# Kernel optimization log

Measured on AMD Instinct MI355X. Metric: run time of the kernel, lower is better.

The kernel has to match this reference:

```python
import jax, jax.numpy as jnp
import numpy as np

C = 0.01          # ToPoincare curvature hardcoded in get_dist
K = 5             # k_way (s0..s4 hardcoded in source)
N = 5             # n_shot
Q = 15            # queries per class -> LQ = K*Q = 75
D = 1024          # feature dim (hardcoded reshape(1,-1,1024))
TEMP = 1.0
N_AUG = 40
MIN_NORM = 1e-5


def _artanh(x):
    return jnp.arctanh(jnp.clip(x, -1 + 1e-5, 1 - 1e-5))


def _project(x, c):
    norm = jnp.maximum(jnp.linalg.norm(x, axis=-1, keepdims=True), MIN_NORM)
    maxnorm = (1 - 1e-3) / jnp.sqrt(c)
    return jnp.where(norm > maxnorm, x / norm * maxnorm, x)


def _expmap0(u, c):
    sc = jnp.sqrt(c)
    un = jnp.maximum(jnp.linalg.norm(u, axis=-1, keepdims=True), MIN_NORM)
    return jnp.tanh(sc * un) * u / (sc * un)


def _mobius_add(x, y, c):
    x2 = jnp.sum(x * x, -1, keepdims=True)
    y2 = jnp.sum(y * y, -1, keepdims=True)
    xy = jnp.sum(x * y, -1, keepdims=True)
    num = (1 + 2 * c * xy + c * y2) * x + (1 - c * x2) * y
    den = 1 + 2 * c * xy + c * c * x2 * y2
    return num / jnp.maximum(den, MIN_NORM)


def _expmap(x, u, c):
    # exp map at point x of tangent vector u
    sc = jnp.sqrt(c)
    un = jnp.maximum(jnp.linalg.norm(u, axis=-1, keepdims=True), MIN_NORM)
    lam = 2.0 / jnp.maximum(1 - c * jnp.sum(x * x, -1, keepdims=True), MIN_NORM)
    second = jnp.tanh(sc * lam * un / 2) * u / (sc * un)
    return _mobius_add(x, second, c)


def _ptransp0_p(x, v, c):
    # parallel transport of v from the origin to x
    return v * (1 - c * jnp.sum(x * x, -1, keepdims=True))


def _dist_matrix(x, y, c):
    # pairwise Poincare distance [n, m] without materializing [n,m,d]:
    # ||(-x) (+) y||^2 = a^2 x2 + b^2 y2 - 2ab<x,y>, a = 1-2c<x,y>+c y2, b = 1-c x2
    sc = jnp.sqrt(c)
    x2 = jnp.sum(x * x, -1)[:, None]
    y2 = jnp.sum(y * y, -1)[None, :]
    xy = x @ y.T
    a = 1 - 2 * c * xy + c * y2
    b = 1 - c * x2
    num2 = a * a * x2 + b * b * y2 - 2 * a * b * xy
    den = 1 - 2 * c * xy + c * c * x2 * y2
    norm = jnp.sqrt(jnp.maximum(num2, 0.0)) / jnp.maximum(den, MIN_NORM)
    return 2.0 / sc * _artanh(sc * norm)


def _p2k(x, c):
    return 2 * x / (1 + c * jnp.sum(x * x, -1, keepdims=True))


def _k2p(x, c):
    return x / (1 + jnp.sqrt(jnp.maximum(1 - c * jnp.sum(x * x, -1, keepdims=True), 0.0)))


def _poincare_mean_masked(x, mask, c):
    # Einstein-midpoint Poincare mean over rows of x weighted by {0,1} mask
    k = _p2k(x, c)
    lam = 1.0 / jnp.sqrt(jnp.maximum(1 - c * jnp.sum(k * k, -1), MIN_NORM))
    w = lam * mask
    mean_k = (w[:, None] * k).sum(0) / w.sum()
    return _k2p(mean_k, c)


def setup_inputs() -> dict:
    key = jax.random.key(0)
    k1, k2, k3 = jax.random.split(key, 3)
    feat = jax.random.normal(k1, (K * N + K * Q, D), dtype=jnp.float32)
    label = jax.random.randint(k2, (2, K * Q), 0, K)
    noise = jax.random.normal(k3, (K, N_AUG, D), dtype=jnp.float32)
    return {"feat": feat, "label": label, "noise": noise}


def reference(feat, label, noise):
    support_e = feat[: N * K].reshape(K, N, D)
    queries_e = feat[N * K:]                                  # [LQ, D]
    support_p_ = _project(_expmap0(feat[: N * K], C), C).reshape(K, N, D)
    queries_p = _project(_expmap0(queries_e, C), C)           # [LQ, D]

    ones_n = jnp.ones((N,), feat.dtype)
    proto_p = jax.vmap(lambda s: _poincare_mean_masked(s, ones_n, C))(support_p_)  # [K, D]
    dist = _dist_matrix(queries_p, proto_p, C) / TEMP          # [LQ, K]
    pred = jnp.argmax(-dist, 1)                                # [LQ]
    qmask = (pred[:, None] == jnp.arange(K)[None, :]).astype(feat.dtype)  # [LQ, K]

    def per_class(sup_p, sup_e, mq, nz):
        # sup_p/sup_e: [N,D]; mq: [LQ] routing mask; nz: [N_AUG,D] unit normals
        m = jnp.concatenate([ones_n, mq])                      # [N+LQ]
        pts_p = jnp.concatenate([sup_p, queries_p], 0)
        pts_e = jnp.concatenate([sup_e, queries_e], 0)
        s_p = _poincare_mean_masked(pts_p, m, C)               # [D] augmented proto
        cnt = m.sum()
        mu = (m[:, None] * pts_e).sum(0) / cnt
        var = (m[:, None] * (pts_e - mu) ** 2).sum(0) / (cnt - 1)  # unbiased, as torch.std
        std = jnp.sqrt(var)                                    # [D]
        v = nz * std                                           # torch.normal(0, std), 40 samples
        pt = _ptransp0_p(s_p[None, :], v, C)
        ex = _expmap(s_p[None, :], pt, C)                      # [N_AUG, D]
        s_new = jnp.concatenate([sup_p, ex], 0)                # [N+N_AUG, D]
        return _poincare_mean_masked(s_new, jnp.ones((N + N_AUG,), feat.dtype), C)

    proto_new = jax.vmap(per_class, in_axes=(0, 0, 1, 0))(support_p_, support_e, qmask, noise)
    dist_new = _dist_matrix(queries_p, proto_new, C) / TEMP

    y_pred = jax.nn.softmax(-dist_new, axis=1)
    log_p_y = jax.nn.log_softmax(-dist, axis=1)
    # nn.CrossEntropyLoss applied to log-probs (double log-softmax, faithful to source)
    ll = jax.nn.log_softmax(log_p_y, axis=1)
    lbl = label[1]
    loss = -jnp.mean(jnp.take_along_axis(ll, lbl[:, None], axis=1))
    return y_pred, loss
```

## Files before the change

### kernel.cpp

```cpp
#include <hip/hip_runtime.h>
#include <hip/hip_bf16.h>
#include <math.h>

#define CCd     0.01
#define SCd     0.1
#define MAXNRMd 9.99
#define MINNd   1e-5
#define DD      1024
#define NK      25
#define NQ      75
#define NROWS   100
#define KCLS    5
#define NAUG    40

__device__ __forceinline__ double wave_reduce_d(double v){
#pragma unroll
  for (int o = 32; o > 0; o >>= 1) v += __shfl_xor(v, o);
  return v;
}

__device__ __forceinline__ double hyp_dist_d(double xy, double x2, double y2){
  double a    = 1.0 - 2.0*CCd*xy + CCd*y2;
  double b    = 1.0 - CCd*x2;
  double num2 = a*a*x2 + b*b*y2 - 2.0*a*b*xy;
  double den  = 1.0 - 2.0*CCd*xy + CCd*CCd*x2*y2;
  double nrm  = sqrt(fmax(num2, 0.0)) / fmax(den, MINNd);
  double z    = SCd * nrm;
  z = fmin(fmax(z, -1.0 + MINNd), 1.0 - MINNd);
  return 10.0 * log((1.0 + z) / (1.0 - z));
}

__device__ __forceinline__ void kweights(double pp, double* la, double* l_out){
  double a  = 2.0/(1.0 + CCd*pp);
  double k2 = a*a*pp;
  double l  = 1.0/sqrt(fmax(1.0 - CCd*k2, MINNd));
  *la = l*a; *l_out = l;
}

__global__ __launch_bounds__(256)
void k_expmap(const float* __restrict__ feat, float* __restrict__ P,
              double* __restrict__ p2d){
  const int r = blockIdx.x, t = threadIdx.x;
  const float4 v = reinterpret_cast<const float4*>(feat + r*DD)[t];
  double ss = (double)v.x*v.x + (double)v.y*v.y + (double)v.z*v.z + (double)v.w*v.w;
  __shared__ double red[4];
  ss = wave_reduce_d(ss);
  if ((t & 63) == 0) red[t >> 6] = ss;
  __syncthreads();
  ss = red[0] + red[1] + red[2] + red[3];
  double un = fmax(sqrt(ss), MINNd);
  double th = tanh(SCd*un);
  double na = th * 10.0;
  double factor, pn;
  if (na > MAXNRMd) { factor = MAXNRMd/un; pn = MAXNRMd; }
  else              { factor = th/(SCd*un); pn = na; }
  float4 o;
  o.x = (float)(v.x*factor); o.y = (float)(v.y*factor);
  o.z = (float)(v.z*factor); o.w = (float)(v.w*factor);
  reinterpret_cast<float4*>(P + r*DD)[t] = o;
  if (t == 0) p2d[r] = pn*pn;
}

__global__ __launch_bounds__(1024)
void k_proto(const float* __restrict__ P, const double* __restrict__ p2d,
             float* __restrict__ protoP, double* __restrict__ proto2d){
  const int c = blockIdx.x, t = threadIdx.x;
  double la[5], wsum = 0.0;
#pragma unroll
  for (int i = 0; i < 5; i++){
    double lam;
    kweights(p2d[c*5+i], &la[i], &lam);
    wsum += lam;
  }
  double s = 0.0;
#pragma unroll
  for (int i = 0; i < 5; i++) s += la[i]*(double)P[(c*5+i)*DD + t];
  s /= wsum;
  __shared__ double red[16];
  double ss = wave_reduce_d(s*s);
  if ((t & 63) == 0) red[t >> 6] = ss;
  __syncthreads();
  ss = 0.0;
#pragma unroll
  for (int i = 0; i < 16; i++) ss += red[i];
  double sf = 1.0/(1.0 + sqrt(fmax(1.0 - CCd*ss, 0.0)));
  protoP[c*DD + t] = (float)(s*sf);
  if (t == 0) proto2d[c] = ss*sf*sf;
}

__global__ __launch_bounds__(256)
void k_dist1(const float* __restrict__ P, const float* __restrict__ protoP,
             const double* __restrict__ p2d, const double* __restrict__ proto2d,
             double* __restrict__ distS, int* __restrict__ predS){
  const int q = blockIdx.x, t = threadIdx.x;
  const float* xq = P + (NK+q)*DD;
  double acc[5] = {0,0,0,0,0};
#pragma unroll
  for (int k = 0; k < 4; k++){
    int d = t + 256*k;
    double x = (double)xq[d];
#pragma unroll
    for (int c = 0; c < 5; c++) acc[c] += x*(double)protoP[c*DD + d];
  }
  __shared__ double red[4][5];
#pragma unroll
  for (int c = 0; c < 5; c++) acc[c] = wave_reduce_d(acc[c]);
  if ((t & 63) == 0){
#pragma unroll
    for (int c = 0; c < 5; c++) red[t >> 6][c] = acc[c];
  }
  __syncthreads();
  if (t == 0){
    double x2 = p2d[NK+q];
    double best = 1e300; int bi = 0;
#pragma unroll
    for (int c = 0; c < 5; c++){
      double dot = red[0][c] + red[1][c] + red[2][c] + red[3][c];
      double dv  = hyp_dist_d(dot, x2, proto2d[c]);
      distS[q*5 + c] = dv;
      if (dv < best){ best = dv; bi = c; }
    }
    predS[q] = bi;
  }
}

__global__ __launch_bounds__(256)
void k_stats(const float* __restrict__ feat, const float* __restrict__ P,
             const double* __restrict__ p2d, const int* __restrict__ predS,
             double* __restrict__ std_g, double* __restrict__ mkr_g,
             double* __restrict__ mk2part){
  const int c = blockIdx.x >> 2, chunk = blockIdx.x & 3, t = threadIdx.x;
  __shared__ double wA[80], wL[80], wM[80], scal[2], red[4];
  __shared__ int rows[80];
  if (t < 80){
    int row; double m;
    if (t < 5){ row = c*5 + t; m = 1.0; }
    else      { row = NK + (t-5); m = (predS[t-5] == c) ? 1.0 : 0.0; }
    rows[t] = row;
    double la, l; kweights(p2d[row], &la, &l);
    wA[t] = m*la; wL[t] = m*l; wM[t] = m;
  }
  __syncthreads();
  if (t == 0){
    double wsum = 0.0, cnt = 0.0;
    for (int i = 0; i < 80; i++){ wsum += wL[i]; cnt += wM[i]; }
    scal[0] = wsum; scal[1] = cnt;
  }
  __syncthreads();
  const double wsum = scal[0], cnt = scal[1];
  const int d = chunk*256 + t;
  double mkd = 0.0, mud = 0.0, sqd = 0.0;
  for (int i = 0; i < 80; i++){
    int row = rows[i];
    mkd += wA[i]*(double)P[row*DD + d];
    double e = (double)feat[row*DD + d];
    mud += wM[i]*e;
    sqd += wM[i]*e*e;
  }
  mkd /= wsum;
  mud /= cnt;
  double var = (sqd - cnt*mud*mud)/(cnt - 1.0);
  std_g[c*DD + d] = sqrt(fmax(var, 0.0));
  mkr_g[c*DD + d] = mkd;
  double s = wave_reduce_d(mkd*mkd);
  if ((t & 63) == 0) red[t >> 6] = s;
  __syncthreads();
  if (t == 0) mk2part[blockIdx.x] = red[0] + red[1] + red[2] + red[3];
}

__global__ __launch_bounds__(256)
void k_coef(const float* __restrict__ noise, const double* __restrict__ std_g,
            const double* __restrict__ mkr_g, const double* __restrict__ mk2part,
            double* __restrict__ coefS_g, double* __restrict__ coefV_g,
            double* __restrict__ lamJ_g){
  const int j = blockIdx.x, c = blockIdx.y, t = threadIdx.x;
  const float*  nzr = noise + (c*NAUG + j)*DD;
  const double* st  = std_g + c*DD;
  const double* mk  = mkr_g + c*DD;
  double un2 = 0.0, rd = 0.0;
#pragma unroll
  for (int k = 0; k < 4; k++){
    int d = t + 256*k;
    double v = (double)nzr[d]*st[d];
    un2 += v*v;
    rd  += v*mk[d];
  }
  __shared__ double red[4][2];
  un2 = wave_reduce_d(un2);
  rd  = wave_reduce_d(rd);
  if ((t & 63) == 0){ red[t >> 6][0] = un2; red[t >> 6][1] = rd; }
  __syncthreads();
  if (t == 0){
    double s_un2 = red[0][0]+red[1][0]+red[2][0]+red[3][0];
    double rdot  = red[0][1]+red[1][1]+red[2][1]+red[3][1];
    double mk2 = mk2part[c*4+0]+mk2part[c*4+1]+mk2part[c*4+2]+mk2part[c*4+3];
    double sf  = 1.0/(1.0 + sqrt(fmax(1.0 - CCd*mk2, 0.0)));
    double sp2 = mk2*sf*sf;
    double lamx = 2.0/fmax(1.0 - CCd*sp2, MINNd);
    double ptf  = 1.0 - CCd*sp2;
    double s_dot = sf*rdot;
    double unv = sqrt(s_un2);
    double unp = fmax(ptf*unv, MINNd);
    double g0  = tanh(SCd*lamx*unp*0.5)/(SCd*unp);
    double g   = g0*ptf;
    double y2  = g*g*s_un2;
    double xy  = g*s_dot;
    double A   = 1.0 + 2.0*CCd*xy + CCd*y2;
    double B   = ptf;
    double den = fmax(1.0 + 2.0*CCd*xy + CCd*CCd*sp2*y2, MINNd);
    double ex2 = (A*A*sp2 + 2.0*A*B*g*s_dot + B*B*g*g*s_un2)/(den*den);
    double ae  = 2.0/(1.0 + CCd*ex2);
    double k2e = ae*ae*ex2;
    double le  = 1.0/sqrt(fmax(1.0 - CCd*k2e, MINNd));
    coefS_g[c*NAUG + j] = le*ae*A/den;
    coefV_g[c*NAUG + j] = le*ae*B*g/den;
    lamJ_g[c*NAUG + j]  = le;
  }
}

__global__ __launch_bounds__(256)
void k_asm(const float* __restrict__ noise, const float* __restrict__ P,
           const double* __restrict__ p2d, const double* __restrict__ std_g,
           const double* __restrict__ mkr_g, const double* __restrict__ mk2part,
           const double* __restrict__ coefS_g, const double* __restrict__ coefV_g,
           const double* __restrict__ lamJ_g,
           float* __restrict__ protoNr, double* __restrict__ mk2Np){
  const int c = blockIdx.x >> 2, chunk = blockIdx.x & 3, t = threadIdx.x;
  __shared__ double cV[NAUG], supC[5], scal[3], red[4];
  if (t < NAUG) cV[t] = coefV_g[c*NAUG + t];
  if (t == 0){
    double lsum = 0.0, sS = 0.0;
#pragma unroll
    for (int i = 0; i < 5; i++){
      double la, l; kweights(p2d[c*5+i], &la, &l);
      supC[i] = la; lsum += l;
    }
    for (int j = 0; j < NAUG; j++){ lsum += lamJ_g[c*NAUG+j]; sS += coefS_g[c*NAUG+j]; }
    double mk2 = mk2part[c*4+0]+mk2part[c*4+1]+mk2part[c*4+2]+mk2part[c*4+3];
    double sf  = 1.0/(1.0 + sqrt(fmax(1.0 - CCd*mk2, 0.0)));
    scal[0] = lsum; scal[1] = sS; scal[2] = sf;
  }
  __syncthreads();
  const int d = chunk*256 + t;
  double val = scal[1]*scal[2]*mkr_g[c*DD + d];
#pragma unroll
  for (int i = 0; i < 5; i++) val += supC[i]*(double)P[(c*5+i)*DD + d];
  double na = 0.0;
  for (int j = 0; j < NAUG; j++) na += cV[j]*(double)noise[(c*NAUG + j)*DD + d];
  val += std_g[c*DD + d]*na;
  val /= scal[0];
  protoNr[c*DD + d] = (float)val;
  double s = wave_reduce_d(val*val);
  if ((t & 63) == 0) red[t >> 6] = s;
  __syncthreads();
  if (t == 0) mk2Np[blockIdx.x] = red[0] + red[1] + red[2] + red[3];
}

__global__ __launch_bounds__(256)
void k_dist2(const float* __restrict__ P, const float* __restrict__ protoNr,
             const double* __restrict__ p2d, const double* __restrict__ mk2Np,
             const double* __restrict__ distS, const int* __restrict__ label,
             float* __restrict__ out, double* __restrict__ lossQ){
  const int q = blockIdx.x, t = threadIdx.x;
  const float* xq = P + (NK+q)*DD;
  double acc[5] = {0,0,0,0,0};
#pragma unroll
  for (int k = 0; k < 4; k++){
    int d = t + 256*k;
    double x = (double)xq[d];
#pragma unroll
    for (int c = 0; c < 5; c++) acc[c] += x*(double)protoNr[c*DD + d];
  }
  __shared__ double red[4][5];
#pragma unroll
  for (int c = 0; c < 5; c++) acc[c] = wave_reduce_d(acc[c]);
  if ((t & 63) == 0){
#pragma unroll
    for (int c = 0; c < 5; c++) red[t >> 6][c] = acc[c];
  }
  __syncthreads();
  if (t == 0){
    double x2 = p2d[NK+q];
    double v[5]; double mx = -1e300;
#pragma unroll
    for (int c = 0; c < 5; c++){
      double mk2N = mk2Np[c*4+0]+mk2Np[c*4+1]+mk2Np[c*4+2]+mk2Np[c*4+3];
      double sfN  = 1.0/(1.0 + sqrt(fmax(1.0 - CCd*mk2N, 0.0)));
      double dot  = sfN*(red[0][c] + red[1][c] + red[2][c] + red[3][c]);
      double y2   = mk2N*sfN*sfN;
      v[c] = -hyp_dist_d(dot, x2, y2);
      mx = fmax(mx, v[c]);
    }
    double se = 0.0;
#pragma unroll
    for (int c = 0; c < 5; c++){ v[c] = exp(v[c]-mx); se += v[c]; }
    double inv = 1.0/se;
#pragma unroll
    for (int c = 0; c < 5; c++) out[q*5 + c] = (float)(v[c]*inv);

    double u[5]; mx = -1e300;
#pragma unroll
    for (int c = 0; c < 5; c++){ u[c] = -distS[q*5+c]; mx = fmax(mx, u[c]); }
    double s1 = 0.0;
#pragma unroll
    for (int c = 0; c < 5; c++) s1 += exp(u[c]-mx);
    double lse1 = mx + log(s1);
#pragma unroll
    for (int c = 0; c < 5; c++) u[c] -= lse1;
    double mx2 = -1e300;
#pragma unroll
    for (int c = 0; c < 5; c++) mx2 = fmax(mx2, u[c]);
    double s2 = 0.0;
#pragma unroll
    for (int c = 0; c < 5; c++) s2 += exp(u[c]-mx2);
    double lse2 = mx2 + log(s2);
    lossQ[q] = u[label[NQ + q]] - lse2;
  }
}

__global__ __launch_bounds__(128)
void k_loss(const double* __restrict__ lossQ, float* __restrict__ out){
  const int t = threadIdx.x;
  double v = (t < NQ) ? lossQ[t] : 0.0;
  v = wave_reduce_d(v);
  __shared__ double red[2];
  if ((t & 63) == 0) red[t >> 6] = v;
  __syncthreads();
  if (t == 0) out[NQ*KCLS] = (float)(-(red[0]+red[1])/75.0);
}

extern "C" void kernel_launch(void* const* d_in, const int* in_sizes, int n_in,
                              void* d_out, int out_size, void* d_ws, size_t ws_size,
                              hipStream_t stream) {
  const float* feat  = (const float*)d_in[0];
  const int*   label = (const int*)d_in[1];
  const float* noise = (const float*)d_in[2];
  float* out = (float*)d_out;

  float*  P        = (float*)d_ws;
  float*  protoP   = P + NROWS*DD;
  float*  protoNr  = protoP + KCLS*DD;
  double* p2d      = (double*)(protoNr + KCLS*DD);
  double* proto2d  = p2d + NROWS;
  double* distS    = proto2d + KCLS;
  double* lossQ    = distS + NQ*KCLS;
  double* std_g    = lossQ + NQ;
  double* mkr_g    = std_g + KCLS*DD;
  double* mk2part  = mkr_g + KCLS*DD;
  double* coefS_g  = mk2part + 4*KCLS;
  double* coefV_g  = coefS_g + KCLS*NAUG;
  double* lamJ_g   = coefV_g + KCLS*NAUG;
  double* mk2Np    = lamJ_g + KCLS*NAUG;
  int*    predS    = (int*)(mk2Np + 4*KCLS);

  k_expmap<<<NROWS, 256, 0, stream>>>(feat, P, p2d);
  k_proto <<<KCLS, 1024, 0, stream>>>(P, p2d, protoP, proto2d);
  k_dist1 <<<NQ, 256, 0, stream>>>(P, protoP, p2d, proto2d, distS, predS);
  k_stats <<<4*KCLS, 256, 0, stream>>>(feat, P, p2d, predS, std_g, mkr_g, mk2part);
  k_coef  <<<dim3(NAUG, KCLS), 256, 0, stream>>>(noise, std_g, mkr_g, mk2part,
                                                 coefS_g, coefV_g, lamJ_g);
  k_asm   <<<4*KCLS, 256, 0, stream>>>(noise, P, p2d, std_g, mkr_g, mk2part,
                                       coefS_g, coefV_g, lamJ_g, protoNr, mk2Np);
  k_dist2 <<<NQ, 256, 0, stream>>>(P, protoNr, p2d, mk2Np, distS, label, out, lossQ);
  k_loss  <<<1, 128, 0, stream>>>(lossQ, out);
}
```

Baseline: 98.29 us.

## Fuse all stages into one cooperative kernel with grid syncs

Replaces the eight separate kernel launches with a single cooperative kernel of 200 blocks that runs each stage in turn, separated by grid.sync(). The prototype computation is also folded into the first distance stage: each query block recomputes the class means and their norms instead of reading a stored prototype. This removes launch overhead and inter-kernel gaps. In exchange it adds grid-wide barrier cost, redundant prototype work in every query block, and a dependence on all 200 blocks being co-resident.

```diff
diff --git a/kernel.cpp b/kernel.cpp
--- a/kernel.cpp
+++ b/kernel.cpp
@@ -1,6 +1,8 @@
 #include <hip/hip_runtime.h>
-#include <hip/hip_bf16.h>
+#include <hip/hip_cooperative_groups.h>
 #include <math.h>
+
+namespace cg = cooperative_groups;
 
 #define CCd     0.01
 #define SCd     0.1
@@ -12,6 +14,7 @@
 #define NROWS   100
 #define KCLS    5
 #define NAUG    40
+#define GRIDB   200
 
 __device__ __forceinline__ double wave_reduce_d(double v){
 #pragma unroll
@@ -38,295 +41,286 @@
 }
 
 __global__ __launch_bounds__(256)
-void k_expmap(const float* __restrict__ feat, float* __restrict__ P,
-              double* __restrict__ p2d){
-  const int r = blockIdx.x, t = threadIdx.x;
-  const float4 v = reinterpret_cast<const float4*>(feat + r*DD)[t];
-  double ss = (double)v.x*v.x + (double)v.y*v.y + (double)v.z*v.z + (double)v.w*v.w;
-  __shared__ double red[4];
-  ss = wave_reduce_d(ss);
-  if ((t & 63) == 0) red[t >> 6] = ss;
-  __syncthreads();
-  ss = red[0] + red[1] + red[2] + red[3];
-  double un = fmax(sqrt(ss), MINNd);
-  double th = tanh(SCd*un);
-  double na = th * 10.0;
-  double factor, pn;
-  if (na > MAXNRMd) { factor = MAXNRMd/un; pn = MAXNRMd; }
-  else              { factor = th/(SCd*un); pn = na; }
-  float4 o;
-  o.x = (float)(v.x*factor); o.y = (float)(v.y*factor);
-  o.z = (float)(v.z*factor); o.w = (float)(v.w*factor);
-  reinterpret_cast<float4*>(P + r*DD)[t] = o;
-  if (t == 0) p2d[r] = pn*pn;
-}
-
-__global__ __launch_bounds__(1024)
-void k_proto(const float* __restrict__ P, const double* __restrict__ p2d,
-             float* __restrict__ protoP, double* __restrict__ proto2d){
-  const int c = blockIdx.x, t = threadIdx.x;
-  double la[5], wsum = 0.0;
-#pragma unroll
-  for (int i = 0; i < 5; i++){
-    double lam;
-    kweights(p2d[c*5+i], &la[i], &lam);
-    wsum += lam;
-  }
-  double s = 0.0;
-#pragma unroll
-  for (int i = 0; i < 5; i++) s += la[i]*(double)P[(c*5+i)*DD + t];
-  s /= wsum;
-  __shared__ double red[16];
-  double ss = wave_reduce_d(s*s);
-  if ((t & 63) == 0) red[t >> 6] = ss;
-  __syncthreads();
-  ss = 0.0;
-#pragma unroll
-  for (int i = 0; i < 16; i++) ss += red[i];
-  double sf = 1.0/(1.0 + sqrt(fmax(1.0 - CCd*ss, 0.0)));
-  protoP[c*DD + t] = (float)(s*sf);
-  if (t == 0) proto2d[c] = ss*sf*sf;
-}
-
-__global__ __launch_bounds__(256)
-void k_dist1(const float* __restrict__ P, const float* __restrict__ protoP,
-             const double* __restrict__ p2d, const double* __restrict__ proto2d,
-             double* __restrict__ distS, int* __restrict__ predS){
-  const int q = blockIdx.x, t = threadIdx.x;
-  const float* xq = P + (NK+q)*DD;
-  double acc[5] = {0,0,0,0,0};
-#pragma unroll
-  for (int k = 0; k < 4; k++){
-    int d = t + 256*k;
-    double x = (double)xq[d];
-#pragma unroll
-    for (int c = 0; c < 5; c++) acc[c] += x*(double)protoP[c*DD + d];
-  }
-  __shared__ double red[4][5];
-#pragma unroll
-  for (int c = 0; c < 5; c++) acc[c] = wave_reduce_d(acc[c]);
-  if ((t & 63) == 0){
-#pragma unroll
-    for (int c = 0; c < 5; c++) red[t >> 6][c] = acc[c];
-  }
-  __syncthreads();
-  if (t == 0){
-    double x2 = p2d[NK+q];
-    double best = 1e300; int bi = 0;
+void k_fused(const float* __restrict__ feat, const int* __restrict__ label,
+             const float* __restrict__ noise, float* __restrict__ out,
+             float* __restrict__ wsf)
+{
+  cg::grid_group grid = cg::this_grid();
+  const int bid = blockIdx.x, t = threadIdx.x;
+  const int lane = t & 63, wv = t >> 6;
+
+  float*  P       = wsf;
+  float*  protoNr = P + NROWS*DD;
+  double* p2d     = (double*)(protoNr + KCLS*DD);
+  double* distS   = p2d + NROWS;
+  double* lossQ   = distS + NQ*KCLS;
+  double* std_g   = lossQ + NQ;
+  double* mkr_g   = std_g + KCLS*DD;
+  double* mk2part = mkr_g + KCLS*DD;
+  double* coefS_g = mk2part + 32;
+  double* coefV_g = coefS_g + KCLS*NAUG;
+  double* lamJ_g  = coefV_g + KCLS*NAUG;
+  double* mk2Np   = lamJ_g + KCLS*NAUG;
+  int*    predS   = (int*)(mk2Np + 32);
+
+  __shared__ double redA[4];
+  __shared__ double redB[4][10];
+  __shared__ double sWA[80], sWL[80], sWM[80];
+  __shared__ int    sRows[80];
+  __shared__ double sScal[4];
+  __shared__ double redD[4][2];
+  __shared__ double sCV[NAUG], sSup[5];
+  __shared__ double redF[4][5];
+
+  if (bid < NROWS){
+    const int r = bid;
+    const float4 v = reinterpret_cast<const float4*>(feat + r*DD)[t];
+    double ss = (double)v.x*v.x + (double)v.y*v.y + (double)v.z*v.z + (double)v.w*v.w;
+    ss = wave_reduce_d(ss);
+    if (lane == 0) redA[wv] = ss;
+    __syncthreads();
+    ss = redA[0] + redA[1] + redA[2] + redA[3];
+    double un = fmax(sqrt(ss), MINNd);
+    double th = tanh(SCd*un);
+    double na = th * 10.0;
+    double factor, pn;
+    if (na > MAXNRMd) { factor = MAXNRMd/un; pn = MAXNRMd; }
+    else              { factor = th/(SCd*un); pn = na; }
+    float4 o;
+    o.x = (float)(v.x*factor); o.y = (float)(v.y*factor);
+    o.z = (float)(v.z*factor); o.w = (float)(v.w*factor);
+    reinterpret_cast<float4*>(P + r*DD)[t] = o;
+    if (t == 0) p2d[r] = pn*pn;
+  }
+  grid.sync();
+
+  if (bid < NQ){
+    const int q = bid;
+    const float* xq = P + (NK+q)*DD;
+    double ss[5], rd[5];
 #pragma unroll
     for (int c = 0; c < 5; c++){
-      double dot = red[0][c] + red[1][c] + red[2][c] + red[3][c];
-      double dv  = hyp_dist_d(dot, x2, proto2d[c]);
-      distS[q*5 + c] = dv;
-      if (dv < best){ best = dv; bi = c; }
-    }
-    predS[q] = bi;
-  }
-}
-
-__global__ __launch_bounds__(256)
-void k_stats(const float* __restrict__ feat, const float* __restrict__ P,
-             const double* __restrict__ p2d, const int* __restrict__ predS,
-             double* __restrict__ std_g, double* __restrict__ mkr_g,
-             double* __restrict__ mk2part){
-  const int c = blockIdx.x >> 2, chunk = blockIdx.x & 3, t = threadIdx.x;
-  __shared__ double wA[80], wL[80], wM[80], scal[2], red[4];
-  __shared__ int rows[80];
-  if (t < 80){
-    int row; double m;
-    if (t < 5){ row = c*5 + t; m = 1.0; }
-    else      { row = NK + (t-5); m = (predS[t-5] == c) ? 1.0 : 0.0; }
-    rows[t] = row;
-    double la, l; kweights(p2d[row], &la, &l);
-    wA[t] = m*la; wL[t] = m*l; wM[t] = m;
-  }
-  __syncthreads();
-  if (t == 0){
-    double wsum = 0.0, cnt = 0.0;
-    for (int i = 0; i < 80; i++){ wsum += wL[i]; cnt += wM[i]; }
-    scal[0] = wsum; scal[1] = cnt;
-  }
-  __syncthreads();
-  const double wsum = scal[0], cnt = scal[1];
-  const int d = chunk*256 + t;
-  double mkd = 0.0, mud = 0.0, sqd = 0.0;
-  for (int i = 0; i < 80; i++){
-    int row = rows[i];
-    mkd += wA[i]*(double)P[row*DD + d];
-    double e = (double)feat[row*DD + d];
-    mud += wM[i]*e;
-    sqd += wM[i]*e*e;
-  }
-  mkd /= wsum;
-  mud /= cnt;
-  double var = (sqd - cnt*mud*mud)/(cnt - 1.0);
-  std_g[c*DD + d] = sqrt(fmax(var, 0.0));
-  mkr_g[c*DD + d] = mkd;
-  double s = wave_reduce_d(mkd*mkd);
-  if ((t & 63) == 0) red[t >> 6] = s;
-  __syncthreads();
-  if (t == 0) mk2part[blockIdx.x] = red[0] + red[1] + red[2] + red[3];
-}
-
-__global__ __launch_bounds__(256)
-void k_coef(const float* __restrict__ noise, const double* __restrict__ std_g,
-            const double* __restrict__ mkr_g, const double* __restrict__ mk2part,
-            double* __restrict__ coefS_g, double* __restrict__ coefV_g,
-            double* __restrict__ lamJ_g){
-  const int j = blockIdx.x, c = blockIdx.y, t = threadIdx.x;
-  const float*  nzr = noise + (c*NAUG + j)*DD;
-  const double* st  = std_g + c*DD;
-  const double* mk  = mkr_g + c*DD;
-  double un2 = 0.0, rd = 0.0;
-#pragma unroll
-  for (int k = 0; k < 4; k++){
-    int d = t + 256*k;
-    double v = (double)nzr[d]*st[d];
-    un2 += v*v;
-    rd  += v*mk[d];
-  }
-  __shared__ double red[4][2];
-  un2 = wave_reduce_d(un2);
-  rd  = wave_reduce_d(rd);
-  if ((t & 63) == 0){ red[t >> 6][0] = un2; red[t >> 6][1] = rd; }
-  __syncthreads();
-  if (t == 0){
-    double s_un2 = red[0][0]+red[1][0]+red[2][0]+red[3][0];
-    double rdot  = red[0][1]+red[1][1]+red[2][1]+red[3][1];
-    double mk2 = mk2part[c*4+0]+mk2part[c*4+1]+mk2part[c*4+2]+mk2part[c*4+3];
-    double sf  = 1.0/(1.0 + sqrt(fmax(1.0 - CCd*mk2, 0.0)));
-    double sp2 = mk2*sf*sf;
-    double lamx = 2.0/fmax(1.0 - CCd*sp2, MINNd);
-    double ptf  = 1.0 - CCd*sp2;
-    double s_dot = sf*rdot;
-    double unv = sqrt(s_un2);
-    double unp = fmax(ptf*unv, MINNd);
-    double g0  = tanh(SCd*lamx*unp*0.5)/(SCd*unp);
-    double g   = g0*ptf;
-    double y2  = g*g*s_un2;
-    double xy  = g*s_dot;
-    double A   = 1.0 + 2.0*CCd*xy + CCd*y2;
-    double B   = ptf;
-    double den = fmax(1.0 + 2.0*CCd*xy + CCd*CCd*sp2*y2, MINNd);
-    double ex2 = (A*A*sp2 + 2.0*A*B*g*s_dot + B*B*g*g*s_un2)/(den*den);
-    double ae  = 2.0/(1.0 + CCd*ex2);
-    double k2e = ae*ae*ex2;
-    double le  = 1.0/sqrt(fmax(1.0 - CCd*k2e, MINNd));
-    coefS_g[c*NAUG + j] = le*ae*A/den;
-    coefV_g[c*NAUG + j] = le*ae*B*g/den;
-    lamJ_g[c*NAUG + j]  = le;
-  }
-}
-
-__global__ __launch_bounds__(256)
-void k_asm(const float* __restrict__ noise, const float* __restrict__ P,
-           const double* __restrict__ p2d, const double* __restrict__ std_g,
-           const double* __restrict__ mkr_g, const double* __restrict__ mk2part,
-           const double* __restrict__ coefS_g, const double* __restrict__ coefV_g,
-           const double* __restrict__ lamJ_g,
-           float* __restrict__ protoNr, double* __restrict__ mk2Np){
-  const int c = blockIdx.x >> 2, chunk = blockIdx.x & 3, t = threadIdx.x;
-  __shared__ double cV[NAUG], supC[5], scal[3], red[4];
-  if (t < NAUG) cV[t] = coefV_g[c*NAUG + t];
-  if (t == 0){
-    double lsum = 0.0, sS = 0.0;
-#pragma unroll
-    for (int i = 0; i < 5; i++){
-      double la, l; kweights(p2d[c*5+i], &la, &l);
-      supC[i] = la; lsum += l;
-    }
-    for (int j = 0; j < NAUG; j++){ lsum += lamJ_g[c*NAUG+j]; sS += coefS_g[c*NAUG+j]; }
-    double mk2 = mk2part[c*4+0]+mk2part[c*4+1]+mk2part[c*4+2]+mk2part[c*4+3];
-    double sf  = 1.0/(1.0 + sqrt(fmax(1.0 - CCd*mk2, 0.0)));
-    scal[0] = lsum; scal[1] = sS; scal[2] = sf;
-  }
-  __syncthreads();
-  const int d = chunk*256 + t;
-  double val = scal[1]*scal[2]*mkr_g[c*DD + d];
-#pragma unroll
-  for (int i = 0; i < 5; i++) val += supC[i]*(double)P[(c*5+i)*DD + d];
-  double na = 0.0;
-  for (int j = 0; j < NAUG; j++) na += cV[j]*(double)noise[(c*NAUG + j)*DD + d];
-  val += std_g[c*DD + d]*na;
-  val /= scal[0];
-  protoNr[c*DD + d] = (float)val;
-  double s = wave_reduce_d(val*val);
-  if ((t & 63) == 0) red[t >> 6] = s;
-  __syncthreads();
-  if (t == 0) mk2Np[blockIdx.x] = red[0] + red[1] + red[2] + red[3];
-}
-
-__global__ __launch_bounds__(256)
-void k_dist2(const float* __restrict__ P, const float* __restrict__ protoNr,
-             const double* __restrict__ p2d, const double* __restrict__ mk2Np,
-             const double* __restrict__ distS, const int* __restrict__ label,
-             float* __restrict__ out, double* __restrict__ lossQ){
-  const int q = blockIdx.x, t = threadIdx.x;
-  const float* xq = P + (NK+q)*DD;
-  double acc[5] = {0,0,0,0,0};
-#pragma unroll
-  for (int k = 0; k < 4; k++){
-    int d = t + 256*k;
-    double x = (double)xq[d];
-#pragma unroll
-    for (int c = 0; c < 5; c++) acc[c] += x*(double)protoNr[c*DD + d];
-  }
-  __shared__ double red[4][5];
-#pragma unroll
-  for (int c = 0; c < 5; c++) acc[c] = wave_reduce_d(acc[c]);
-  if ((t & 63) == 0){
-#pragma unroll
-    for (int c = 0; c < 5; c++) red[t >> 6][c] = acc[c];
-  }
-  __syncthreads();
-  if (t == 0){
-    double x2 = p2d[NK+q];
-    double v[5]; double mx = -1e300;
-#pragma unroll
-    for (int c = 0; c < 5; c++){
-      double mk2N = mk2Np[c*4+0]+mk2Np[c*4+1]+mk2Np[c*4+2]+mk2Np[c*4+3];
-      double sfN  = 1.0/(1.0 + sqrt(fmax(1.0 - CCd*mk2N, 0.0)));
-      double dot  = sfN*(red[0][c] + red[1][c] + red[2][c] + red[3][c]);
-      double y2   = mk2N*sfN*sfN;
-      v[c] = -hyp_dist_d(dot, x2, y2);
-      mx = fmax(mx, v[c]);
-    }
-    double se = 0.0;
-#pragma unroll
-    for (int c = 0; c < 5; c++){ v[c] = exp(v[c]-mx); se += v[c]; }
-    double inv = 1.0/se;
-#pragma unroll
-    for (int c = 0; c < 5; c++) out[q*5 + c] = (float)(v[c]*inv);
-
-    double u[5]; mx = -1e300;
-#pragma unroll
-    for (int c = 0; c < 5; c++){ u[c] = -distS[q*5+c]; mx = fmax(mx, u[c]); }
-    double s1 = 0.0;
-#pragma unroll
-    for (int c = 0; c < 5; c++) s1 += exp(u[c]-mx);
-    double lse1 = mx + log(s1);
-#pragma unroll
-    for (int c = 0; c < 5; c++) u[c] -= lse1;
-    double mx2 = -1e300;
-#pragma unroll
-    for (int c = 0; c < 5; c++) mx2 = fmax(mx2, u[c]);
-    double s2 = 0.0;
-#pragma unroll
-    for (int c = 0; c < 5; c++) s2 += exp(u[c]-mx2);
-    double lse2 = mx2 + log(s2);
-    lossQ[q] = u[label[NQ + q]] - lse2;
-  }
-}
-
-__global__ __launch_bounds__(128)
-void k_loss(const double* __restrict__ lossQ, float* __restrict__ out){
-  const int t = threadIdx.x;
-  double v = (t < NQ) ? lossQ[t] : 0.0;
-  v = wave_reduce_d(v);
-  __shared__ double red[2];
-  if ((t & 63) == 0) red[t >> 6] = v;
-  __syncthreads();
-  if (t == 0) out[NQ*KCLS] = (float)(-(red[0]+red[1])/75.0);
+      double la[5], wsum = 0.0;
+#pragma unroll
+      for (int i = 0; i < 5; i++){
+        double lv; kweights(p2d[c*5+i], &la[i], &lv); wsum += lv;
+      }
+      double ssc = 0.0, rdc = 0.0;
+#pragma unroll
+      for (int k = 0; k < 4; k++){
+        int d = t + 256*k;
+        double s = 0.0;
+#pragma unroll
+        for (int i = 0; i < 5; i++) s += la[i]*(double)P[(c*5+i)*DD + d];
+        s /= wsum;
+        ssc += s*s; rdc += s*(double)xq[d];
+      }
+      ss[c] = wave_reduce_d(ssc);
+      rd[c] = wave_reduce_d(rdc);
+    }
+    if (lane == 0){
+#pragma unroll
+      for (int c = 0; c < 5; c++){ redB[wv][c] = ss[c]; redB[wv][5+c] = rd[c]; }
+    }
+    __syncthreads();
+    if (t == 0){
+      double x2 = p2d[NK+q];
+      double best = 1e300; int bi = 0;
+#pragma unroll
+      for (int c = 0; c < 5; c++){
+        double sst = redB[0][c]+redB[1][c]+redB[2][c]+redB[3][c];
+        double rdt = redB[0][5+c]+redB[1][5+c]+redB[2][5+c]+redB[3][5+c];
+        double sf  = 1.0/(1.0 + sqrt(fmax(1.0 - CCd*sst, 0.0)));
+        double dv  = hyp_dist_d(sf*rdt, x2, sst*sf*sf);
+        distS[q*5 + c] = dv;
+        if (dv < best){ best = dv; bi = c; }
+      }
+      predS[q] = bi;
+    }
+  }
+  grid.sync();
+
+  if (bid < 4*KCLS){
+    const int c = bid >> 2, chunk = bid & 3;
+    if (t < 80){
+      int row; double m;
+      if (t < 5){ row = c*5 + t; m = 1.0; }
+      else      { row = NK + (t-5); m = (predS[t-5] == c) ? 1.0 : 0.0; }
+      sRows[t] = row;
+      double la, l; kweights(p2d[row], &la, &l);
+      sWA[t] = m*la; sWL[t] = m*l; sWM[t] = m;
+    }
+    __syncthreads();
+    if (t == 0){
+      double wsum = 0.0, cnt = 0.0;
+      for (int i = 0; i < 80; i++){ wsum += sWL[i]; cnt += sWM[i]; }
+      sScal[0] = wsum; sScal[1] = cnt;
+    }
+    __syncthreads();
+    const double wsum = sScal[0], cnt = sScal[1];
+    const int d = chunk*256 + t;
+    double mkd = 0.0, mud = 0.0, sqd = 0.0;
+    for (int i = 0; i < 80; i++){
+      int row = sRows[i];
+      mkd += sWA[i]*(double)P[row*DD + d];
+      double e = (double)feat[row*DD + d];
+      mud += sWM[i]*e;
+      sqd += sWM[i]*e*e;
+    }
+    mkd /= wsum;
+    mud /= cnt;
+    double var = (sqd - cnt*mud*mud)/(cnt - 1.0);
+    std_g[c*DD + d] = sqrt(fmax(var, 0.0));
+    mkr_g[c*DD + d] = mkd;
+    double s = wave_reduce_d(mkd*mkd);
+    if (lane == 0) redA[wv] = s;
+    __syncthreads();
+    if (t == 0) mk2part[bid] = redA[0] + redA[1] + redA[2] + redA[3];
+  }
+  grid.sync();
+
+  {
+    const int c = bid / NAUG, j = bid % NAUG;
+    const float*  nzr = noise + (c*NAUG + j)*DD;
+    const double* st  = std_g + c*DD;
+    const double* mk  = mkr_g + c*DD;
+    double un2 = 0.0, rdd = 0.0;
+#pragma unroll
+    for (int k = 0; k < 4; k++){
+      int d = t + 256*k;
+      double v = (double)nzr[d]*st[d];
+      un2 += v*v;
+      rdd += v*mk[d];
+    }
+    un2 = wave_reduce_d(un2);
+    rdd = wave_reduce_d(rdd);
+    if (lane == 0){ redD[wv][0] = un2; redD[wv][1] = rdd; }
+    __syncthreads();
+    if (t == 0){
+      double s_un2 = redD[0][0]+redD[1][0]+redD[2][0]+redD[3][0];
+      double rdot  = redD[0][1]+redD[1][1]+redD[2][1]+redD[3][1];
+      double mk2 = mk2part[c*4+0]+mk2part[c*4+1]+mk2part[c*4+2]+mk2part[c*4+3];
+      double sf  = 1.0/(1.0 + sqrt(fmax(1.0 - CCd*mk2, 0.0)));
+      double sp2 = mk2*sf*sf;
+      double lamx = 2.0/fmax(1.0 - CCd*sp2, MINNd);
+      double ptf  = 1.0 - CCd*sp2;
+      double s_dot = sf*rdot;
+      double unv = sqrt(s_un2);
+      double unp = fmax(ptf*unv, MINNd);
+      double g0  = tanh(SCd*lamx*unp*0.5)/(SCd*unp);
+      double g   = g0*ptf;
+      double y2  = g*g*s_un2;
+      double xy  = g*s_dot;
+      double A   = 1.0 + 2.0*CCd*xy + CCd*y2;
+      double B   = ptf;
+      double den = fmax(1.0 + 2.0*CCd*xy + CCd*CCd*sp2*y2, MINNd);
+      double ex2 = (A*A*sp2 + 2.0*A*B*g*s_dot + B*B*g*g*s_un2)/(den*den);
+      double ae  = 2.0/(1.0 + CCd*ex2);
+      double k2e = ae*ae*ex2;
+      double le  = 1.0/sqrt(fmax(1.0 - CCd*k2e, MINNd));
+      coefS_g[c*NAUG + j] = le*ae*A/den;
+      coefV_g[c*NAUG + j] = le*ae*B*g/den;
+      lamJ_g[c*NAUG + j]  = le;
+    }
+  }
+  grid.sync();
+
+  if (bid < 4*KCLS){
+    const int c = bid >> 2, chunk = bid & 3;
+    if (t < NAUG) sCV[t] = coefV_g[c*NAUG + t];
+    if (t == 0){
+      double lsum = 0.0, sS = 0.0;
+#pragma unroll
+      for (int i = 0; i < 5; i++){
+        double la, l; kweights(p2d[c*5+i], &la, &l);
+        sSup[i] = la; lsum += l;
+      }
+      for (int j = 0; j < NAUG; j++){ lsum += lamJ_g[c*NAUG+j]; sS += coefS_g[c*NAUG+j]; }
+      double mk2 = mk2part[c*4+0]+mk2part[c*4+1]+mk2part[c*4+2]+mk2part[c*4+3];
+      double sf  = 1.0/(1.0 + sqrt(fmax(1.0 - CCd*mk2, 0.0)));
+      sScal[0] = lsum; sScal[1] = sS; sScal[2] = sf;
+    }
+    __syncthreads();
+    const int d = chunk*256 + t;
+    double val = sScal[1]*sScal[2]*mkr_g[c*DD + d];
+#pragma unroll
+    for (int i = 0; i < 5; i++) val += sSup[i]*(double)P[(c*5+i)*DD + d];
+    double na = 0.0;
+    for (int j = 0; j < NAUG; j++) na += sCV[j]*(double)noise[(c*NAUG + j)*DD + d];
+    val += std_g[c*DD + d]*na;
+    val /= sScal[0];
+    protoNr[c*DD + d] = (float)val;
+    double s = wave_reduce_d(val*val);
+    if (lane == 0) redA[wv] = s;
+    __syncthreads();
+    if (t == 0) mk2Np[bid] = redA[0] + redA[1] + redA[2] + redA[3];
+  }
+  grid.sync();
+
+  if (bid < NQ){
+    const int q = bid;
+    const float* xq = P + (NK+q)*DD;
+    double acc[5] = {0,0,0,0,0};
+#pragma unroll
+    for (int k = 0; k < 4; k++){
+      int d = t + 256*k;
+      double x = (double)xq[d];
+#pragma unroll
+      for (int c = 0; c < 5; c++) acc[c] += x*(double)protoNr[c*DD + d];
+    }
+#pragma unroll
+    for (int c = 0; c < 5; c++) acc[c] = wave_reduce_d(acc[c]);
+    if (lane == 0){
+#pragma unroll
+      for (int c = 0; c < 5; c++) redF[wv][c] = acc[c];
+    }
+    __syncthreads();
+    if (t == 0){
+      double x2 = p2d[NK+q];
+      double v[5]; double mx = -1e300;
+#pragma unroll
+      for (int c = 0; c < 5; c++){
+        double mk2N = mk2Np[c*4+0]+mk2Np[c*4+1]+mk2Np[c*4+2]+mk2Np[c*4+3];
+        double sfN  = 1.0/(1.0 + sqrt(fmax(1.0 - CCd*mk2N, 0.0)));
+        double dot  = sfN*(redF[0][c]+redF[1][c]+redF[2][c]+redF[3][c]);
+        v[c] = -hyp_dist_d(dot, x2, mk2N*sfN*sfN);
+        mx = fmax(mx, v[c]);
+      }
+      double se = 0.0;
+#pragma unroll
+      for (int c = 0; c < 5; c++){ v[c] = exp(v[c]-mx); se += v[c]; }
+      double inv = 1.0/se;
+#pragma unroll
+      for (int c = 0; c < 5; c++) out[q*5 + c] = (float)(v[c]*inv);
+
+      double u[5]; mx = -1e300;
+#pragma unroll
+      for (int c = 0; c < 5; c++){ u[c] = -distS[q*5+c]; mx = fmax(mx, u[c]); }
+      double s1 = 0.0;
+#pragma unroll
+      for (int c = 0; c < 5; c++) s1 += exp(u[c]-mx);
+      double lse1 = mx + log(s1);
+#pragma unroll
+      for (int c = 0; c < 5; c++) u[c] -= lse1;
+      double mx2 = -1e300;
+#pragma unroll
+      for (int c = 0; c < 5; c++) mx2 = fmax(mx2, u[c]);
+      double s2 = 0.0;
+#pragma unroll
+      for (int c = 0; c < 5; c++) s2 += exp(u[c]-mx2);
+      double lse2 = mx2 + log(s2);
+      lossQ[q] = u[label[NQ + q]] - lse2;
+    }
+  }
+  grid.sync();
+
+  if (bid == 0){
+    double v = (t < NQ) ? lossQ[t] : 0.0;
+    v = wave_reduce_d(v);
+    if (lane == 0) redA[wv] = v;
+    __syncthreads();
+    if (t == 0) out[NQ*KCLS] = (float)(-(redA[0]+redA[1]+redA[2]+redA[3])/75.0);
+  }
 }
 
 extern "C" void kernel_launch(void* const* d_in, const int* in_sizes, int n_in,
@@ -336,31 +330,10 @@
   const int*   label = (const int*)d_in[1];
   const float* noise = (const float*)d_in[2];
   float* out = (float*)d_out;
-
-  float*  P        = (float*)d_ws;
-  float*  protoP   = P + NROWS*DD;
-  float*  protoNr  = protoP + KCLS*DD;
-  double* p2d      = (double*)(protoNr + KCLS*DD);
-  double* proto2d  = p2d + NROWS;
-  double* distS    = proto2d + KCLS;
-  double* lossQ    = distS + NQ*KCLS;
-  double* std_g    = lossQ + NQ;
-  double* mkr_g    = std_g + KCLS*DD;
-  double* mk2part  = mkr_g + KCLS*DD;
-  double* coefS_g  = mk2part + 4*KCLS;
-  double* coefV_g  = coefS_g + KCLS*NAUG;
-  double* lamJ_g   = coefV_g + KCLS*NAUG;
-  double* mk2Np    = lamJ_g + KCLS*NAUG;
-  int*    predS    = (int*)(mk2Np + 4*KCLS);
-
-  k_expmap<<<NROWS, 256, 0, stream>>>(feat, P, p2d);
-  k_proto <<<KCLS, 1024, 0, stream>>>(P, p2d, protoP, proto2d);
-  k_dist1 <<<NQ, 256, 0, stream>>>(P, protoP, p2d, proto2d, distS, predS);
-  k_stats <<<4*KCLS, 256, 0, stream>>>(feat, P, p2d, predS, std_g, mkr_g, mk2part);
-  k_coef  <<<dim3(NAUG, KCLS), 256, 0, stream>>>(noise, std_g, mkr_g, mk2part,
-                                                 coefS_g, coefV_g, lamJ_g);
-  k_asm   <<<4*KCLS, 256, 0, stream>>>(noise, P, p2d, std_g, mkr_g, mk2part,
-                                       coefS_g, coefV_g, lamJ_g, protoNr, mk2Np);
-  k_dist2 <<<NQ, 256, 0, stream>>>(P, protoNr, p2d, mk2Np, distS, label, out, lossQ);
-  k_loss  <<<1, 128, 0, stream>>>(lossQ, out);
-}
+  float* wsf = (float*)d_ws;
+
+  void* args[] = { (void*)&feat, (void*)&label, (void*)&noise,
+                   (void*)&out, (void*)&wsf };
+  hipLaunchCooperativeKernel((const void*)k_fused, dim3(GRIDB), dim3(256),
+                             args, 0, stream);
+}
```

New measurement: 219.1 us. 2.23x slower.

## Fold prototype computation into dist1 and merge loss into dist2 via last-block atomic

Applied to the files above, without the earlier changes.

Drops the k_proto kernel. Each k_dist1 block now recomputes the five class prototypes itself and keeps only the reductions it needs (squared norm and dot with the query), then applies the Klein-to-Poincare scaling scalarly. The k_loss kernel is also removed: the last k_dist2 block, found through an atomic counter reset in k_expmap, does the final mean. This removes two kernel launches and their inter-kernel gaps, at the cost of redundant prototype arithmetic and extra reads of support rows in each of the 75 dist1 blocks.

```diff
diff --git a/kernel.cpp b/kernel.cpp
--- a/kernel.cpp
+++ b/kernel.cpp
@@ -39,8 +39,9 @@
 
 __global__ __launch_bounds__(256)
 void k_expmap(const float* __restrict__ feat, float* __restrict__ P,
-              double* __restrict__ p2d){
+              double* __restrict__ p2d, int* __restrict__ cnt){
   const int r = blockIdx.x, t = threadIdx.x;
+  if (r == 0 && t == 0) *cnt = 0;
   const float4 v = reinterpret_cast<const float4*>(feat + r*DD)[t];
   double ss = (double)v.x*v.x + (double)v.y*v.y + (double)v.z*v.z + (double)v.w*v.w;
   __shared__ double red[4];
@@ -61,53 +62,37 @@
   if (t == 0) p2d[r] = pn*pn;
 }
 
-__global__ __launch_bounds__(1024)
-void k_proto(const float* __restrict__ P, const double* __restrict__ p2d,
-             float* __restrict__ protoP, double* __restrict__ proto2d){
-  const int c = blockIdx.x, t = threadIdx.x;
-  double la[5], wsum = 0.0;
-#pragma unroll
-  for (int i = 0; i < 5; i++){
-    double lam;
-    kweights(p2d[c*5+i], &la[i], &lam);
-    wsum += lam;
-  }
-  double s = 0.0;
-#pragma unroll
-  for (int i = 0; i < 5; i++) s += la[i]*(double)P[(c*5+i)*DD + t];
-  s /= wsum;
-  __shared__ double red[16];
-  double ss = wave_reduce_d(s*s);
-  if ((t & 63) == 0) red[t >> 6] = ss;
-  __syncthreads();
-  ss = 0.0;
-#pragma unroll
-  for (int i = 0; i < 16; i++) ss += red[i];
-  double sf = 1.0/(1.0 + sqrt(fmax(1.0 - CCd*ss, 0.0)));
-  protoP[c*DD + t] = (float)(s*sf);
-  if (t == 0) proto2d[c] = ss*sf*sf;
-}
-
-__global__ __launch_bounds__(256)
-void k_dist1(const float* __restrict__ P, const float* __restrict__ protoP,
-             const double* __restrict__ p2d, const double* __restrict__ proto2d,
+__global__ __launch_bounds__(256)
+void k_dist1(const float* __restrict__ P, const double* __restrict__ p2d,
              double* __restrict__ distS, int* __restrict__ predS){
   const int q = blockIdx.x, t = threadIdx.x;
+  const int lane = t & 63, wv = t >> 6;
   const float* xq = P + (NK+q)*DD;
-  double acc[5] = {0,0,0,0,0};
-#pragma unroll
-  for (int k = 0; k < 4; k++){
-    int d = t + 256*k;
-    double x = (double)xq[d];
-#pragma unroll
-    for (int c = 0; c < 5; c++) acc[c] += x*(double)protoP[c*DD + d];
-  }
-  __shared__ double red[4][5];
-#pragma unroll
-  for (int c = 0; c < 5; c++) acc[c] = wave_reduce_d(acc[c]);
-  if ((t & 63) == 0){
-#pragma unroll
-    for (int c = 0; c < 5; c++) red[t >> 6][c] = acc[c];
+  __shared__ double redB[4][10];
+  double ss[5], rd[5];
+#pragma unroll
+  for (int c = 0; c < 5; c++){
+    double la[5], wsum = 0.0;
+#pragma unroll
+    for (int i = 0; i < 5; i++){
+      double lv; kweights(p2d[c*5+i], &la[i], &lv); wsum += lv;
+    }
+    double ssc = 0.0, rdc = 0.0;
+#pragma unroll
+    for (int k = 0; k < 4; k++){
+      int d = t + 256*k;
+      double s = 0.0;
+#pragma unroll
+      for (int i = 0; i < 5; i++) s += la[i]*(double)P[(c*5+i)*DD + d];
+      s /= wsum;
+      ssc += s*s; rdc += s*(double)xq[d];
+    }
+    ss[c] = wave_reduce_d(ssc);
+    rd[c] = wave_reduce_d(rdc);
+  }
+  if (lane == 0){
+#pragma unroll
+    for (int c = 0; c < 5; c++){ redB[wv][c] = ss[c]; redB[wv][5+c] = rd[c]; }
   }
   __syncthreads();
   if (t == 0){
@@ -115,8 +100,10 @@
     double best = 1e300; int bi = 0;
 #pragma unroll
     for (int c = 0; c < 5; c++){
-      double dot = red[0][c] + red[1][c] + red[2][c] + red[3][c];
-      double dv  = hyp_dist_d(dot, x2, proto2d[c]);
+      double sst = redB[0][c]+redB[1][c]+redB[2][c]+redB[3][c];
+      double rdt = redB[0][5+c]+redB[1][5+c]+redB[2][5+c]+redB[3][5+c];
+      double sf  = 1.0/(1.0 + sqrt(fmax(1.0 - CCd*sst, 0.0)));
+      double dv  = hyp_dist_d(sf*rdt, x2, sst*sf*sf);
       distS[q*5 + c] = dv;
       if (dv < best){ best = dv; bi = c; }
     }
@@ -260,7 +247,8 @@
 void k_dist2(const float* __restrict__ P, const float* __restrict__ protoNr,
              const double* __restrict__ p2d, const double* __restrict__ mk2Np,
              const double* __restrict__ distS, const int* __restrict__ label,
-             float* __restrict__ out, double* __restrict__ lossQ){
+             float* __restrict__ out, double* __restrict__ lossQ,
+             int* __restrict__ cnt){
   const int q = blockIdx.x, t = threadIdx.x;
   const float* xq = P + (NK+q)*DD;
   double acc[5] = {0,0,0,0,0};
@@ -272,6 +260,7 @@
     for (int c = 0; c < 5; c++) acc[c] += x*(double)protoNr[c*DD + d];
   }
   __shared__ double red[4][5];
+  __shared__ int isLast;
 #pragma unroll
   for (int c = 0; c < 5; c++) acc[c] = wave_reduce_d(acc[c]);
   if ((t & 63) == 0){
@@ -287,8 +276,7 @@
       double mk2N = mk2Np[c*4+0]+mk2Np[c*4+1]+mk2Np[c*4+2]+mk2Np[c*4+3];
       double sfN  = 1.0/(1.0 + sqrt(fmax(1.0 - CCd*mk2N, 0.0)));
       double dot  = sfN*(red[0][c] + red[1][c] + red[2][c] + red[3][c]);
-      double y2   = mk2N*sfN*sfN;
-      v[c] = -hyp_dist_d(dot, x2, y2);
+      v[c] = -hyp_dist_d(dot, x2, mk2N*sfN*sfN);
       mx = fmax(mx, v[c]);
     }
     double se = 0.0;
@@ -315,18 +303,20 @@
     for (int c = 0; c < 5; c++) s2 += exp(u[c]-mx2);
     double lse2 = mx2 + log(s2);
     lossQ[q] = u[label[NQ + q]] - lse2;
-  }
-}
-
-__global__ __launch_bounds__(128)
-void k_loss(const double* __restrict__ lossQ, float* __restrict__ out){
-  const int t = threadIdx.x;
-  double v = (t < NQ) ? lossQ[t] : 0.0;
-  v = wave_reduce_d(v);
-  __shared__ double red[2];
-  if ((t & 63) == 0) red[t >> 6] = v;
-  __syncthreads();
-  if (t == 0) out[NQ*KCLS] = (float)(-(red[0]+red[1])/75.0);
+
+    __threadfence();
+    isLast = (atomicAdd(cnt, 1) == NQ - 1) ? 1 : 0;
+  }
+  __syncthreads();
+  if (isLast){
+    __threadfence();
+    double v = (t < NQ) ? lossQ[t] : 0.0;
+    v = wave_reduce_d(v);
+    __shared__ double redL[4];
+    if ((t & 63) == 0) redL[t >> 6] = v;
+    __syncthreads();
+    if (t == 0) out[NQ*KCLS] = (float)(-(redL[0]+redL[1]+redL[2]+redL[3])/75.0);
+  }
 }
 
 extern "C" void kernel_launch(void* const* d_in, const int* in_sizes, int n_in,
@@ -338,29 +328,27 @@
   float* out = (float*)d_out;
 
   float*  P        = (float*)d_ws;
-  float*  protoP   = P + NROWS*DD;
-  float*  protoNr  = protoP + KCLS*DD;
+  float*  protoNr  = P + NROWS*DD;
   double* p2d      = (double*)(protoNr + KCLS*DD);
-  double* proto2d  = p2d + NROWS;
-  double* distS    = proto2d + KCLS;
+  double* distS    = p2d + NROWS;
   double* lossQ    = distS + NQ*KCLS;
   double* std_g    = lossQ + NQ;
   double* mkr_g    = std_g + KCLS*DD;
   double* mk2part  = mkr_g + KCLS*DD;
-  double* coefS_g  = mk2part + 4*KCLS;
+  double* coefS_g  = mk2part + 32;
   double* coefV_g  = coefS_g + KCLS*NAUG;
   double* lamJ_g   = coefV_g + KCLS*NAUG;
   double* mk2Np    = lamJ_g + KCLS*NAUG;
-  int*    predS    = (int*)(mk2Np + 4*KCLS);
-
-  k_expmap<<<NROWS, 256, 0, stream>>>(feat, P, p2d);
-  k_proto <<<KCLS, 1024, 0, stream>>>(P, p2d, protoP, proto2d);
-  k_dist1 <<<NQ, 256, 0, stream>>>(P, protoP, p2d, proto2d, distS, predS);
+  int*    predS    = (int*)(mk2Np + 32);
+  int*    cnt      = predS + NQ;
+
+  k_expmap<<<NROWS, 256, 0, stream>>>(feat, P, p2d, cnt);
+  k_dist1 <<<NQ, 256, 0, stream>>>(P, p2d, distS, predS);
   k_stats <<<4*KCLS, 256, 0, stream>>>(feat, P, p2d, predS, std_g, mkr_g, mk2part);
   k_coef  <<<dim3(NAUG, KCLS), 256, 0, stream>>>(noise, std_g, mkr_g, mk2part,
                                                  coefS_g, coefV_g, lamJ_g);
   k_asm   <<<4*KCLS, 256, 0, stream>>>(noise, P, p2d, std_g, mkr_g, mk2part,
                                        coefS_g, coefV_g, lamJ_g, protoNr, mk2Np);
-  k_dist2 <<<NQ, 256, 0, stream>>>(P, protoNr, p2d, mk2Np, distS, label, out, lossQ);
-  k_loss  <<<1, 128, 0, stream>>>(lossQ, out);
-}
+  k_dist2 <<<NQ, 256, 0, stream>>>(P, protoNr, p2d, mk2Np, distS, label, out,
+                                   lossQ, cnt);
+}
```

Measured after the change: 101.1 us. 2.8% more time.
